# Optimization experiments

Measured on AMD Instinct MI355X. Metric: run time of the kernel, lower is better.

## Reference

```python
import jax, jax.numpy as jnp
import numpy as np
import math

B, TQ, TK, D, H, K = 4, 1024, 1536, 1024, 16, 1
DV = D // H * K  # 64
DP = D * K       # projection dim


def setup_inputs() -> dict:
    key = jax.random.key(0)
    ks = jax.random.split(key, 12)
    s = 0.02
    query = jax.random.normal(ks[0], (B, TQ, D), dtype=jnp.float32)
    key_value = jax.random.normal(ks[1], (B, TK, D), dtype=jnp.float32)
    relative = jax.random.normal(ks[2], (B, TK, D), dtype=jnp.float32)
    # Transformer-XL causal mask: query i may attend to key j <= i + mem
    mem = TK - TQ
    i = jnp.arange(TQ)[:, None]
    j = jnp.arange(TK)[None, :]
    mask = jnp.broadcast_to(j > i + mem, (B, TQ, TK))  # True = masked
    Wq = jax.random.normal(ks[3], (D, DP), dtype=jnp.float32) * s
    Wk = jax.random.normal(ks[4], (D, DP), dtype=jnp.float32) * s
    Wv = jax.random.normal(ks[5], (D, DP), dtype=jnp.float32) * s
    Wr = jax.random.normal(ks[6], (D, DP), dtype=jnp.float32) * s
    Wo = jax.random.normal(ks[7], (DP, D), dtype=jnp.float32) * s
    u = jax.random.normal(ks[8], (DV,), dtype=jnp.float32) * s
    v = jax.random.normal(ks[9], (DV,), dtype=jnp.float32) * s
    gamma = jnp.ones((D,), dtype=jnp.float32)
    beta = jnp.zeros((D,), dtype=jnp.float32)
    return {"query": query, "key_value": key_value, "relative": relative,
            "mask": mask, "Wq": Wq, "Wk": Wk, "Wv": Wv, "Wr": Wr, "Wo": Wo,
            "u": u, "v": v, "gamma": gamma, "beta": beta}


def _layer_norm(x, gamma, beta, eps=1e-5):
    mu = jnp.mean(x, axis=-1, keepdims=True)
    var = jnp.mean(jnp.square(x - mu), axis=-1, keepdims=True)
    return (x - mu) * jax.lax.rsqrt(var + eps) * gamma + beta


def reference(query, key_value, relative, mask, Wq, Wk, Wv, Wr, Wo, u, v, gamma, beta):
    b, tq, d = query.shape
    tk = key_value.shape[1]
    dv = u.shape[0]
    h = Wq.shape[1] // dv
    q = (query @ Wq).reshape(b, tq, h, dv)
    k = (key_value @ Wk).reshape(b, tk, h, dv)
    val = (key_value @ Wv).reshape(b, tk, h, dv)
    r = (relative @ Wr).reshape(b, tk, h, dv)
    # content term (q+u)K^T and position term (q+v)R^T, per head
    ac = jnp.einsum('bqhd,bkhd->bhqk', q + u, k)
    bd = jnp.einsum('bqhd,bkhd->bhqk', q + v, r)
    logits = (ac + bd) * (1.0 / math.sqrt(dv))
    logits = jnp.where(mask[:, None, :, :], -jnp.inf, logits)
    w = jax.nn.softmax(logits, axis=-1)
    ctx = jnp.einsum('bhqk,bkhd->bqhd', w, val).reshape(b, tq, h * dv)
    out = ctx @ Wo + query  # residual
    return _layer_norm(out, gamma, beta)
```

## Files before the change

### kernel.cpp

```cpp
#include <hip/hip_runtime.h>


typedef unsigned short u16;
typedef __attribute__((ext_vector_type(8))) short short8;
typedef __attribute__((ext_vector_type(4))) float floatx4;

__device__ __forceinline__ float bf2f(u16 u) {
    union { unsigned int i; float f; } w; w.i = ((unsigned int)u) << 16; return w.f;
}
__device__ __forceinline__ u16 f2bf(float f) {
    union { unsigned int i; float f; } w; w.f = f;
    unsigned int u = w.i;
    return (u16)((u + 0x7FFFu + ((u >> 16) & 1u)) >> 16);
}

__device__ __forceinline__ void gl_lds16(const u16* g, u16* lds) {
    __builtin_amdgcn_global_load_lds(
        (const __attribute__((address_space(1))) void*)g,
        (__attribute__((address_space(3))) void*)lds, 16, 0, 0);
}

__global__ __launch_bounds__(256) void cvt3_kernel(
    const float* __restrict__ x0, u16* __restrict__ y0, int n0,
    const float* __restrict__ x1, u16* __restrict__ y1, int n1,
    const float* __restrict__ x2, u16* __restrict__ y2, int n2)
{
    const int which = blockIdx.y;
    const float* x = (which == 0) ? x0 : (which == 1) ? x1 : x2;
    u16* y         = (which == 0) ? y0 : (which == 1) ? y1 : y2;
    const int n    = (which == 0) ? n0 : (which == 1) ? n1 : n2;
    const int i = (blockIdx.x * 256 + threadIdx.x) * 8;
    if (i >= n) return;
    float4 a = *(const float4*)&x[i];
    float4 b = *(const float4*)&x[i + 4];
    short8 o;
    o[0] = (short)f2bf(a.x); o[1] = (short)f2bf(a.y);
    o[2] = (short)f2bf(a.z); o[3] = (short)f2bf(a.w);
    o[4] = (short)f2bf(b.x); o[5] = (short)f2bf(b.y);
    o[6] = (short)f2bf(b.z); o[7] = (short)f2bf(b.w);
    *(short8*)&y[i] = o;
}

__global__ __launch_bounds__(256) void transpose5_kernel(
    const float* __restrict__ Wq, const float* __restrict__ Wk,
    const float* __restrict__ Wr, const float* __restrict__ Wv,
    const float* __restrict__ Wo,
    u16* __restrict__ WqT, u16* __restrict__ WkrT,
    u16* __restrict__ WvT, u16* __restrict__ WoT)
{
    const int z = blockIdx.z;
    const float* W; u16* WT; int dst_ld, dst_koff;
    switch (z) {
        case 0: W = Wq; WT = WqT;  dst_ld = 1024; dst_koff = 0;    break;
        case 1: W = Wk; WT = WkrT; dst_ld = 2048; dst_koff = 0;    break;
        case 2: W = Wr; WT = WkrT; dst_ld = 2048; dst_koff = 1024; break;
        case 3: W = Wv; WT = WvT;  dst_ld = 1024; dst_koff = 0;    break;
        default:W = Wo; WT = WoT;  dst_ld = 1024; dst_koff = 0;    break;
    }
    __shared__ u16 ts[64][72];
    const int k0 = blockIdx.x * 64, n0 = blockIdx.y * 64;
    const int r  = threadIdx.x >> 2;
    const int c4 = (threadIdx.x & 3) << 4;
    const float* src = &W[(size_t)(k0 + r) * 1024 + n0 + c4];
    for (int j = 0; j < 16; j += 4) {
        float4 a = *(const float4*)(src + j);
        ts[r][c4 + j + 0] = f2bf(a.x);
        ts[r][c4 + j + 1] = f2bf(a.y);
        ts[r][c4 + j + 2] = f2bf(a.z);
        ts[r][c4 + j + 3] = f2bf(a.w);
    }
    __syncthreads();
    short8 t0, t1;
    for (int j = 0; j < 8; j++) t0[j] = (short)ts[c4 + j][r];
    for (int j = 0; j < 8; j++) t1[j] = (short)ts[c4 + 8 + j][r];
    u16* dst = &WT[(size_t)(n0 + r) * dst_ld + dst_koff + k0 + c4];
    *(short8*)dst       = t0;
    *(short8*)(dst + 8) = t1;
}

__global__ __launch_bounds__(256) void wuv_kernel(
    const float* __restrict__ Wk, const float* __restrict__ Wr,
    const float* __restrict__ u, const float* __restrict__ v,
    u16* __restrict__ wuvb)
{
    int idx = blockIdx.x * 256 + threadIdx.x;
    int c = idx >> 4, h = idx & 15;
    float au = 0.f, av = 0.f;
    for (int d = 0; d < 64; d++) {
        au += Wk[(size_t)c * 1024 + h * 64 + d] * u[d];
        av += Wr[(size_t)c * 1024 + h * 64 + d] * v[d];
    }
    wuvb[h * 2048 + c]        = f2bf(au);
    wuvb[h * 2048 + 1024 + c] = f2bf(av);
}

template <int EPI>
__device__ __forceinline__ void gemm_body(
    const u16* __restrict__ A0, const u16* __restrict__ A1,
    const u16* __restrict__ WT, void* __restrict__ out,
    int Kld, int kbeg, int kend, int Ksplit, int T,
    int bm, int bn, u16* As, u16* Ws)
{
    const int tid = threadIdx.x;
    const int wave = tid >> 6, lane = tid & 63;
    const int wm = wave >> 1, wn = wave & 1;
    const int l16 = lane & 15, quad = lane >> 4;

    floatx4 acc[4][4];
    const floatx4 zf = {0.f, 0.f, 0.f, 0.f};
    for (int i = 0; i < 4; i++) for (int j = 0; j < 4; j++) acc[i][j] = zf;

    const int m_base = bm * 128, n_base = bn * 128;
    const int rl = lane >> 2;
    const int cl = (lane & 3) * 8;

    for (int k0 = kbeg; k0 < kend; k0 += 32) {
        const u16* Aptr; int kk;
        if (k0 < Ksplit) { Aptr = A0; kk = k0; } else { Aptr = A1; kk = k0 - Ksplit; }
        __syncthreads();
        for (int half = 0; half < 2; half++) {
            const int r = wave * 32 + half * 16;
            gl_lds16(Aptr + (size_t)(m_base + r + rl) * 1024 + kk + cl, &As[r * 32]);
            gl_lds16(WT   + (size_t)(n_base + r + rl) * Kld  + k0 + cl, &Ws[r * 32]);
        }
        __syncthreads();

        short8 af[4], bf[4];
        for (int i = 0; i < 4; i++) {
            af[i] = *(const short8*)&As[(wm * 64 + i * 16 + l16) * 32 + quad * 8];
            bf[i] = *(const short8*)&Ws[(wn * 64 + i * 16 + l16) * 32 + quad * 8];
        }
        for (int i = 0; i < 4; i++)
            for (int j = 0; j < 4; j++)
                acc[i][j] = __builtin_amdgcn_mfma_f32_16x16x32_bf16(af[i], bf[j], acc[i][j], 0, 0, 0);
    }

    for (int i = 0; i < 4; i++) {
        for (int rg = 0; rg < 4; rg++) {
            const int m = m_base + wm * 64 + i * 16 + quad * 4 + rg;
            if (EPI == 0) {
                const int b = m / T, t = m % T;
                u16* op = (u16*)out;
                for (int j = 0; j < 4; j++) {
                    const int col = n_base + wn * 64 + j * 16 + l16;
                    const int h = col >> 6, d = col & 63;
                    op[((((size_t)b * 16 + h) * T + t) << 6) + d] = f2bf(acc[i][j][rg]);
                }
            } else if (EPI == 2) {
                const int b = m / T, t = m % T;
                u16* op = (u16*)out;
                for (int j = 0; j < 4; j++) {
                    const int col = n_base + wn * 64 + j * 16 + l16;
                    const int h = col >> 6, d = col & 63;
                    op[(((size_t)b * 16 + h) * 64 + d) * 1536 + t] = f2bf(acc[i][j][rg]);
                }
            } else {
                float* op = (float*)out;
                for (int j = 0; j < 4; j++) {
                    const int col = n_base + wn * 64 + j * 16 + l16;
                    op[(size_t)m * 1024 + col] = acc[i][j][rg];
                }
            }
        }
    }
}

__device__ __forceinline__ void bias_body(
    const u16* __restrict__ kvb, const u16* __restrict__ relb,
    const u16* __restrict__ wuvb, float* __restrict__ bias, int bblk)
{
    const int tid = threadIdx.x;
    const int wave = tid >> 6, lane = tid & 63;
    const int l16 = lane & 15, quad = lane >> 4;
    const int tBase = bblk * 64 + wave * 16;

    floatx4 acc = {0.f, 0.f, 0.f, 0.f};
    const u16* arow_kv  = kvb  + (size_t)(tBase + l16) * 1024;
    const u16* arow_rel = relb + (size_t)(tBase + l16) * 1024;
    const u16* brow     = wuvb + (size_t)l16 * 2048;

    for (int ks = 0; ks < 64; ks++) {
        const int k0 = ks * 32;
        const u16* ap = (k0 < 1024) ? (arow_kv + k0) : (arow_rel + k0 - 1024);
        short8 af = *(const short8*)(ap + quad * 8);
        short8 bf = *(const short8*)(brow + k0 + quad * 8);
        acc = __builtin_amdgcn_mfma_f32_16x16x32_bf16(af, bf, acc, 0, 0, 0);
    }
    for (int rg = 0; rg < 4; rg++) {
        const int tg = tBase + quad * 4 + rg;
        const int b = tg / 1536, t = tg % 1536;
        bias[((size_t)b * 16 + l16) * 1536 + t] = acc[rg];
    }
}

__global__ __launch_bounds__(256) void fused_proj(
    const u16* __restrict__ qb, const u16* __restrict__ kvb,
    const u16* __restrict__ relb,
    const u16* __restrict__ WqT, const u16* __restrict__ WkrT,
    const u16* __restrict__ WvT, const u16* __restrict__ wuvb,
    u16* __restrict__ Qh, u16* __restrict__ KRh, u16* __restrict__ Vt,
    float* __restrict__ bias)
{
    __shared__ u16 smem[2 * 128 * 32];
    u16* As = smem;
    u16* Ws = smem + 128 * 32;
    const int blk = blockIdx.x;
    if (blk < 384) {
        gemm_body<0>(kvb, relb, WkrT, KRh, 2048, 0, 2048, 1024, 1536,
                     blk % 48, blk / 48, As, Ws);
    } else if (blk < 768) {
        const int i = blk - 384;
        gemm_body<2>(kvb, nullptr, WvT, Vt, 1024, 0, 1024, 1024, 1536,
                     i % 48, i / 48, As, Ws);
    } else if (blk < 1024) {
        const int i = blk - 768;
        gemm_body<0>(qb, nullptr, WqT, Qh, 1024, 0, 1024, 1024, 1024,
                     i % 32, i / 32, As, Ws);
    } else {
        bias_body(kvb, relb, wuvb, bias, blk - 1024);
    }
}

__global__ __launch_bounds__(256) void out_gemm(
    const u16* __restrict__ ctx, const u16* __restrict__ WoT,
    float* __restrict__ outp)
{
    __shared__ u16 smem[2 * 128 * 32];
    const int z = blockIdx.z;
    gemm_body<3>(ctx, nullptr, WoT,
                 outp + (size_t)z * 4 * 1024 * 1024, 1024,
                 z * 512, z * 512 + 512, 1024, 1024,
                 blockIdx.x, blockIdx.y, smem, smem + 128 * 32);
}

__global__ __launch_bounds__(256) void attn_kernel(
    const u16* __restrict__ Qh,
    const u16* __restrict__ KRh,
    const u16* __restrict__ Vt,
    const float* __restrict__ bias,
    u16* __restrict__ ctx)
{
    const int blk  = blockIdx.x;
    const int hb   = blk & 63;
    const int qblk = blk >> 6;
    const int b = hb >> 4, h = hb & 15;
    const int tid = threadIdx.x;
    const int wave = tid >> 6, lane = tid & 63;
    const int l16 = lane & 15, quad = lane >> 4;
    const int q0 = qblk * 128;

    const u16* Qp = Qh  + (size_t)hb * 1024 * 64;
    const u16* Kp = KRh + (size_t)hb * 1536 * 64;
    const u16* Vp = Vt  + (size_t)hb * 64 * 1536;
    const float* bp = bias + (size_t)hb * 1536;

    __shared__ u16 Ps[4][2][16][68];

    short8 aq[2][2];
    for (int mi = 0; mi < 2; mi++)
        for (int ks = 0; ks < 2; ks++)
            aq[mi][ks] = *(const short8*)
                &Qp[(size_t)(q0 + wave * 32 + mi * 16 + l16) * 64 + ks * 32 + quad * 8];

    const floatx4 zf = {0.f, 0.f, 0.f, 0.f};
    floatx4 accO[2][4];
    float lsum[2][4];
    for (int mi = 0; mi < 2; mi++)
        for (int j = 0; j < 4; j++) accO[mi][j] = zf;
    for (int mi = 0; mi < 2; mi++)
        for (int rg = 0; rg < 4; rg++) lsum[mi][rg] = 0.f;

    const int nkt = 2 * qblk + 10;
    for (int kt = 0; kt < nkt; kt++) {
        const int k0 = kt * 64;

        short8 bk[4][2], bv[4][2];
        float bcol[4];
        for (int n = 0; n < 4; n++)
            for (int ks = 0; ks < 2; ks++)
                bk[n][ks] = *(const short8*)
                    &Kp[(size_t)(k0 + n * 16 + l16) * 64 + ks * 32 + quad * 8];
        for (int j = 0; j < 4; j++)
            for (int ks = 0; ks < 2; ks++)
                bv[j][ks] = *(const short8*)
                    &Vp[(size_t)(j * 16 + l16) * 1536 + k0 + ks * 32 + quad * 8];
        for (int n = 0; n < 4; n++) bcol[n] = bp[k0 + n * 16 + l16];

        const bool domask = (k0 + 63 > q0 + 512);

        for (int mi = 0; mi < 2; mi++) {
            floatx4 accS[4];
            for (int n = 0; n < 4; n++) {
                accS[n] = zf;
                for (int ks = 0; ks < 2; ks++)
                    accS[n] = __builtin_amdgcn_mfma_f32_16x16x32_bf16(
                        aq[mi][ks], bk[n][ks], accS[n], 0, 0, 0);
            }
            const int qrow = q0 + wave * 32 + mi * 16 + quad * 4;
            for (int n = 0; n < 4; n++) {
                const int col = k0 + n * 16 + l16;
                for (int rg = 0; rg < 4; rg++) {
                    float s = (accS[n][rg] + bcol[n]) * 0.125f;
                    if (domask && col > qrow + rg + 512) s = -1e30f;
                    const float p = __expf(s);
                    lsum[mi][rg] += p;
                    Ps[wave][mi][quad * 4 + rg][n * 16 + l16] = f2bf(p);
                }
            }
            short8 ap[2];
            for (int ks = 0; ks < 2; ks++)
                ap[ks] = *(const short8*)&Ps[wave][mi][l16][ks * 32 + quad * 8];
            for (int j = 0; j < 4; j++)
                for (int ks = 0; ks < 2; ks++)
                    accO[mi][j] = __builtin_amdgcn_mfma_f32_16x16x32_bf16(
                        ap[ks], bv[j][ks], accO[mi][j], 0, 0, 0);
        }
    }

    for (int mi = 0; mi < 2; mi++)
        for (int rg = 0; rg < 4; rg++) {
            float s = lsum[mi][rg];
            for (int off = 1; off < 16; off <<= 1) s += __shfl_xor(s, off, 64);
            lsum[mi][rg] = s;
        }

    for (int mi = 0; mi < 2; mi++)
        for (int j = 0; j < 4; j++)
            for (int rg = 0; rg < 4; rg++) {
                const int q = q0 + wave * 32 + mi * 16 + quad * 4 + rg;
                const int d = j * 16 + l16;
                ctx[((size_t)b * 1024 + q) * 1024 + h * 64 + d] =
                    f2bf(accO[mi][j][rg] / lsum[mi][rg]);
            }
}

__global__ __launch_bounds__(256) void ln_kernel(
    const float* __restrict__ x0, const float* __restrict__ x1,
    const float* __restrict__ q,
    const float* __restrict__ gamma, const float* __restrict__ beta,
    float* __restrict__ out)
{
    const int row = blockIdx.x;
    const int tid = threadIdx.x;
    const size_t base = (size_t)row * 1024 + tid * 4;
    float4 a = *(const float4*)&x0[base];
    float4 c = *(const float4*)&x1[base];
    float4 r = *(const float4*)&q[base];
    float4 v;
    v.x = a.x + c.x + r.x; v.y = a.y + c.y + r.y;
    v.z = a.z + c.z + r.z; v.w = a.w + c.w + r.w;
    float s  = v.x + v.y + v.z + v.w;
    float ss = v.x * v.x + v.y * v.y + v.z * v.z + v.w * v.w;
    for (int off = 1; off < 64; off <<= 1) {
        s  += __shfl_xor(s, off, 64);
        ss += __shfl_xor(ss, off, 64);
    }
    __shared__ float sm[8];
    const int wave = tid >> 6, lane = tid & 63;
    if (lane == 0) { sm[wave] = s; sm[4 + wave] = ss; }
    __syncthreads();
    s  = sm[0] + sm[1] + sm[2] + sm[3];
    ss = sm[4] + sm[5] + sm[6] + sm[7];
    const float mu  = s * (1.f / 1024.f);
    const float var = ss * (1.f / 1024.f) - mu * mu;
    const float inv = rsqrtf(var + 1e-5f);
    float* op = out + (size_t)row * 1024;
    const float* ve = &v.x;
    for (int j = 0; j < 4; j++) {
        const int c2 = tid * 4 + j;
        op[c2] = (ve[j] - mu) * inv * gamma[c2] + beta[c2];
    }
}

extern "C" void kernel_launch(void* const* d_in, const int* in_sizes, int n_in,
                              void* d_out, int out_size, void* d_ws, size_t ws_size,
                              hipStream_t stream)
{
    const float* query     = (const float*)d_in[0];
    const float* key_value = (const float*)d_in[1];
    const float* relative  = (const float*)d_in[2];
    const float* Wq = (const float*)d_in[4];
    const float* Wk = (const float*)d_in[5];
    const float* Wv = (const float*)d_in[6];
    const float* Wr = (const float*)d_in[7];
    const float* Wo = (const float*)d_in[8];
    const float* u  = (const float*)d_in[9];
    const float* v  = (const float*)d_in[10];
    const float* gamma = (const float*)d_in[11];
    const float* beta  = (const float*)d_in[12];

    char* wsp = (char*)d_ws;
    auto alloc = [&](size_t bytes) -> char* {
        char* p = wsp; wsp += (bytes + 255) & ~(size_t)255; return p;
    };
    u16*   qb   = (u16*)alloc((size_t)4 * 1024 * 1024 * 2);
    u16*   kvb  = (u16*)alloc((size_t)4 * 1536 * 1024 * 2);
    u16*   relb = (u16*)alloc((size_t)4 * 1536 * 1024 * 2);
    u16*   WqT  = (u16*)alloc((size_t)1024 * 1024 * 2);
    u16*   WkrT = (u16*)alloc((size_t)1024 * 2048 * 2);
    u16*   WvT  = (u16*)alloc((size_t)1024 * 1024 * 2);
    u16*   WoT  = (u16*)alloc((size_t)1024 * 1024 * 2);
    u16*   wuvb = (u16*)alloc((size_t)16 * 2048 * 2);
    u16*   Qh   = (u16*)alloc((size_t)4 * 16 * 1024 * 64 * 2);
    u16*   KRh  = (u16*)alloc((size_t)4 * 16 * 1536 * 64 * 2);
    u16*   Vt   = (u16*)alloc((size_t)4 * 16 * 64 * 1536 * 2);
    float* bias = (float*)alloc((size_t)4 * 16 * 1536 * 4);
    u16*   ctx  = (u16*)alloc((size_t)4 * 1024 * 1024 * 2);
    float* outp = (float*)alloc((size_t)2 * 4 * 1024 * 1024 * 4);

    const dim3 tb(256);
    cvt3_kernel<<<dim3(3072, 3), tb, 0, stream>>>(
        query, qb, 4 * 1024 * 1024,
        key_value, kvb, 4 * 1536 * 1024,
        relative, relb, 4 * 1536 * 1024);

    transpose5_kernel<<<dim3(16, 16, 5), tb, 0, stream>>>(
        Wq, Wk, Wr, Wv, Wo, WqT, WkrT, WvT, WoT);
    wuv_kernel<<<64, tb, 0, stream>>>(Wk, Wr, u, v, wuvb);

    fused_proj<<<dim3(1120), tb, 0, stream>>>(
        qb, kvb, relb, WqT, WkrT, WvT, wuvb, Qh, KRh, Vt, bias);

    attn_kernel<<<dim3(512), tb, 0, stream>>>(Qh, KRh, Vt, bias, ctx);

    out_gemm<<<dim3(32, 8, 2), tb, 0, stream>>>(ctx, WoT, outp);
    ln_kernel<<<4096, tb, 0, stream>>>(
        outp, outp + (size_t)4 * 1024 * 1024, query, gamma, beta, (float*)d_out);
}
```

Baseline: 345.3 us.

## Split attention over two key chunks with a combine kernel; swizzle GEMM LDS

The attention kernel now splits each query block's key range into two halves and runs them as separate blocks. Each block writes unnormalized fp32 partial outputs and row sums, and a new combine kernel adds the two halves, normalizes, and writes bf16 ctx. This doubles the grid to improve CU occupancy and load balance on the causal workload, at the cost of an extra kernel launch and fp32 partial traffic. The partials reuse workspace buffers that are dead by then. The GEMM body also XOR-swizzles the LDS column chunks on both write and read to reduce bank conflicts in the fragment loads.

```diff
diff --git a/kernel.cpp b/kernel.cpp
--- a/kernel.cpp
+++ b/kernel.cpp
@@ -112,7 +112,8 @@
 
     const int m_base = bm * 128, n_base = bn * 128;
     const int rl = lane >> 2;
-    const int cl = (lane & 3) * 8;
+    const int cswz = (((lane & 3) ^ ((lane >> 3) & 3)) << 3);
+    const int rsd  = ((quad ^ ((l16 >> 1) & 3)) << 3);
 
     for (int k0 = kbeg; k0 < kend; k0 += 32) {
         const u16* Aptr; int kk;
@@ -120,15 +121,15 @@
         __syncthreads();
         for (int half = 0; half < 2; half++) {
             const int r = wave * 32 + half * 16;
-            gl_lds16(Aptr + (size_t)(m_base + r + rl) * 1024 + kk + cl, &As[r * 32]);
-            gl_lds16(WT   + (size_t)(n_base + r + rl) * Kld  + k0 + cl, &Ws[r * 32]);
+            gl_lds16(Aptr + (size_t)(m_base + r + rl) * 1024 + kk + cswz, &As[r * 32]);
+            gl_lds16(WT   + (size_t)(n_base + r + rl) * Kld  + k0 + cswz, &Ws[r * 32]);
         }
         __syncthreads();
 
         short8 af[4], bf[4];
         for (int i = 0; i < 4; i++) {
-            af[i] = *(const short8*)&As[(wm * 64 + i * 16 + l16) * 32 + quad * 8];
-            bf[i] = *(const short8*)&Ws[(wn * 64 + i * 16 + l16) * 32 + quad * 8];
+            af[i] = *(const short8*)&As[(wm * 64 + i * 16 + l16) * 32 + rsd];
+            bf[i] = *(const short8*)&Ws[(wn * 64 + i * 16 + l16) * 32 + rsd];
         }
         for (int i = 0; i < 4; i++)
             for (int j = 0; j < 4; j++)
@@ -238,12 +239,14 @@
     const u16* __restrict__ KRh,
     const u16* __restrict__ Vt,
     const float* __restrict__ bias,
-    u16* __restrict__ ctx)
+    float* __restrict__ Opart,
+    float* __restrict__ Lpart)
 {
     const int blk  = blockIdx.x;
     const int hb   = blk & 63;
-    const int qblk = blk >> 6;
-    const int b = hb >> 4, h = hb & 15;
+    const int rest = blk >> 6;
+    const int qblk = rest & 7;
+    const int kchunk = rest >> 3;
     const int tid = threadIdx.x;
     const int wave = tid >> 6, lane = tid & 63;
     const int l16 = lane & 15, quad = lane >> 4;
@@ -270,8 +273,12 @@
     for (int mi = 0; mi < 2; mi++)
         for (int rg = 0; rg < 4; rg++) lsum[mi][rg] = 0.f;
 
-    const int nkt = 2 * qblk + 10;
-    for (int kt = 0; kt < nkt; kt++) {
+    const int nkt  = 2 * qblk + 10;
+    const int half = (nkt + 1) >> 1;
+    const int kt_beg = kchunk ? half : 0;
+    const int kt_end = kchunk ? nkt : half;
+
+    for (int kt = kt_beg; kt < kt_end; kt++) {
         const int k0 = kt * 64;
 
         short8 bk[4][2], bv[4][2];
@@ -324,14 +331,37 @@
             lsum[mi][rg] = s;
         }
 
-    for (int mi = 0; mi < 2; mi++)
+    float* Op = Opart + ((size_t)(kchunk * 64 + hb) * 1024) * 64;
+    float* Lp = Lpart + (size_t)(kchunk * 64 + hb) * 1024;
+    for (int mi = 0; mi < 2; mi++) {
         for (int j = 0; j < 4; j++)
             for (int rg = 0; rg < 4; rg++) {
                 const int q = q0 + wave * 32 + mi * 16 + quad * 4 + rg;
-                const int d = j * 16 + l16;
-                ctx[((size_t)b * 1024 + q) * 1024 + h * 64 + d] =
-                    f2bf(accO[mi][j][rg] / lsum[mi][rg]);
+                Op[(size_t)q * 64 + j * 16 + l16] = accO[mi][j][rg];
             }
+        if (l16 == 0)
+            for (int rg = 0; rg < 4; rg++)
+                Lp[q0 + wave * 32 + mi * 16 + quad * 4 + rg] = lsum[mi][rg];
+    }
+}
+
+__global__ __launch_bounds__(256) void attn_combine(
+    const float* __restrict__ Opart, const float* __restrict__ Lpart,
+    u16* __restrict__ ctx)
+{
+    const size_t i4 = ((size_t)blockIdx.x * 256 + threadIdx.x) * 4;
+    float4 a = *(const float4*)&Opart[i4];
+    float4 c = *(const float4*)&Opart[(size_t)64 * 1024 * 64 + i4];
+    const int hbq = (int)(i4 >> 6);
+    const float inv = 1.f / (Lpart[hbq] + Lpart[64 * 1024 + hbq]);
+    const int hb = hbq >> 10, q = hbq & 1023;
+    const int b = hb >> 4, h = hb & 15;
+    const int d = (int)(i4 & 63);
+    u16* op = &ctx[((size_t)b * 1024 + q) * 1024 + h * 64 + d];
+    op[0] = f2bf((a.x + c.x) * inv);
+    op[1] = f2bf((a.y + c.y) * inv);
+    op[2] = f2bf((a.z + c.z) * inv);
+    op[3] = f2bf((a.w + c.w) * inv);
 }
 
 __global__ __launch_bounds__(256) void ln_kernel(
@@ -408,6 +438,9 @@
     u16*   ctx  = (u16*)alloc((size_t)4 * 1024 * 1024 * 2);
     float* outp = (float*)alloc((size_t)2 * 4 * 1024 * 1024 * 4);
 
+    float* Opart = (float*)qb;
+    float* Lpart = Opart + (size_t)2 * 64 * 1024 * 64;
+
     const dim3 tb(256);
     cvt3_kernel<<<dim3(3072, 3), tb, 0, stream>>>(
         query, qb, 4 * 1024 * 1024,
@@ -421,7 +454,8 @@
     fused_proj<<<dim3(1120), tb, 0, stream>>>(
         qb, kvb, relb, WqT, WkrT, WvT, wuvb, Qh, KRh, Vt, bias);
 
-    attn_kernel<<<dim3(512), tb, 0, stream>>>(Qh, KRh, Vt, bias, ctx);
+    attn_kernel<<<dim3(1024), tb, 0, stream>>>(Qh, KRh, Vt, bias, Opart, Lpart);
+    attn_combine<<<dim3(4096), tb, 0, stream>>>(Opart, Lpart, ctx);
 
     out_gemm<<<dim3(32, 8, 2), tb, 0, stream>>>(ctx, WoT, outp);
     ln_kernel<<<4096, tb, 0, stream>>>(
```

After: 349.9 us. No clear change (+1.3%).
